# Performance work log

Measured on AMD Instinct MI355X. Metric: run time of the kernel, lower is better.

The kernel has to match this reference:

```python
import jax, jax.numpy as jnp
import numpy as np

B, T, C = 2, 2048, 1024
NH = 16
HD = C // NH

def setup_inputs() -> dict:
    key = jax.random.key(0)
    ks = jax.random.split(key, 4)
    x = jax.random.normal(ks[0], (B, T, C), dtype=jnp.float32)
    w_attn = jax.random.normal(ks[1], (C, 3 * C), dtype=jnp.float32) * (1.0 / np.sqrt(C))
    b_attn = jnp.zeros((3 * C,), dtype=jnp.float32)
    w_proj = jax.random.normal(ks[2], (C, C), dtype=jnp.float32) * (1.0 / np.sqrt(C))
    b_proj = jnp.zeros((C,), dtype=jnp.float32)
    return {"x": x, "w_attn": w_attn, "b_attn": b_attn, "w_proj": w_proj, "b_proj": b_proj}

def reference(x, w_attn, b_attn, w_proj, b_proj):
    Bq, Tq, Cq = x.shape
    qkv = x @ w_attn + b_attn                      # [B,T,3C]
    q, k, v = jnp.split(qkv, 3, axis=2)
    # [B,T,C] -> [B,NH,T,HD]
    def heads(t):
        return t.reshape(Bq, Tq, NH, HD).transpose(0, 2, 1, 3)
    q, k, v = heads(q), heads(k), heads(v)
    att = jnp.einsum('bhqd,bhkd->bhqk', q, k) * (1.0 / np.sqrt(HD))
    causal = jnp.tril(jnp.ones((Tq, Tq), dtype=bool))
    att = jnp.where(causal[None, None], att, -jnp.inf)
    att = jax.nn.softmax(att, axis=-1)
    y = jnp.einsum('bhqk,bhkd->bhqd', att, v)      # [B,NH,T,HD]
    y = y.transpose(0, 2, 1, 3).reshape(Bq, Tq, Cq)
    return y @ w_proj + b_proj
```

## Files before the change

### kernel.cpp

```cpp
#include <hip/hip_runtime.h>

typedef unsigned short u16;
typedef short bf16x8 __attribute__((ext_vector_type(8)));
typedef float f32x4 __attribute__((ext_vector_type(4)));
typedef float f32x16 __attribute__((ext_vector_type(16)));

#define BATCH 2
#define SEQ   2048
#define CH    1024
#define NHEAD 16
#define HDIM  64
#define ROWS  (BATCH*SEQ)

#define WAITV(N) asm volatile("s_waitcnt vmcnt(" #N ")" ::: "memory")

__device__ __forceinline__ u16 f2b(float f) {
  unsigned u = __builtin_bit_cast(unsigned, f);
  u += 0x7FFFu + ((u >> 16) & 1u);
  return (u16)(u >> 16);
}
__device__ __forceinline__ float b2f(u16 h) {
  unsigned u = ((unsigned)h) << 16;
  return __builtin_bit_cast(float, u);
}
__device__ __forceinline__ float exp2_fast(float x) {
  float r; asm("v_exp_f32 %0, %1" : "=v"(r) : "v"(x)); return r;
}
__device__ __forceinline__ unsigned cvt_pk_bf16(float a, float b) {
  unsigned r; asm("v_cvt_pk_bf16_f32 %0, %1, %2" : "=v"(r) : "v"(a), "v"(b)); return r;
}

__device__ __forceinline__ void gload_lds16(const void* g, void* l) {
  __builtin_amdgcn_global_load_lds(
      (const __attribute__((address_space(1))) unsigned int*)g,
      (__attribute__((address_space(3))) unsigned int*)l, 16, 0, 0);
}

__global__ void csa_prep(const float* __restrict__ x,
                         const float* __restrict__ wa, const float* __restrict__ wp,
                         u16* __restrict__ xb, u16* __restrict__ wat,
                         u16* __restrict__ wpt) {
  __shared__ float tile[32][33];
  const int b = blockIdx.x, t = threadIdx.x;
  if (b < 2048) {
    int i = b * 256 + t;
    const float4* f4 = (const float4*)x;
    float4 v0 = f4[2*i], v1 = f4[2*i+1];
    ushort4 o0, o1;
    o0.x = f2b(v0.x); o0.y = f2b(v0.y); o0.z = f2b(v0.z); o0.w = f2b(v0.w);
    o1.x = f2b(v1.x); o1.y = f2b(v1.y); o1.z = f2b(v1.z); o1.w = f2b(v1.w);
    ((ushort4*)xb)[2*i]   = o0;
    ((ushort4*)xb)[2*i+1] = o1;
    return;
  }
  int bb = b - 2048;
  int bx = bb & 127, by = bb >> 7;
  const float* in; u16* out; int C;
  if (bx < 96) { in = wa; out = wat; C = 3*CH; }
  else         { in = wp; out = wpt; C = CH; bx -= 96; }
  const int R = CH;
  const int bxc = bx * 32, byc = by * 32;
  const int tx = t & 31, ty = t >> 5;
  #pragma unroll
  for (int j = 0; j < 4; ++j) {
    int r = byc + ty + j*8, c = bxc + tx;
    tile[ty + j*8][tx] = in[(size_t)r*C + c];
  }
  __syncthreads();
  #pragma unroll
  for (int j = 0; j < 4; ++j) {
    int oc = bxc + ty + j*8;
    int orr = byc + tx;
    out[(size_t)oc*R + orr] = f2b(tile[tx][ty + j*8]);
  }
}

__global__ __launch_bounds__(512) void csa_gemm_qkv(
    const u16* __restrict__ A, const u16* __restrict__ Bt,
    const float* __restrict__ bias,
    u16* __restrict__ qbo, u16* __restrict__ kb, u16* __restrict__ vtb)
{
  __shared__ __align__(16) u16 As[3][256*64];
  __shared__ __align__(16) u16 Bs[2][192*64];
  const int t = threadIdx.x, lane = t & 63, w = t >> 6;
  const int wm = w >> 2, wn = w & 3, g = lane >> 4, qi = lane & 15;
  const int xq = (qi & 7) * 8;

  const int wgid = blockIdx.y * 16 + blockIdx.x;
  const int c8 = wgid & 7, inner = wgid >> 3;
  const int bm = (c8 >> 1) * 4 + (inner >> 3);
  const int bn = (c8 & 1) * 8 + (inner & 7);

  f32x4 acc[8][3] = {};

  const u16* Ab = A  + (size_t)(bm*256)*CH;
  const u16* Bb = Bt + (size_t)(bn*192)*CH;
  const int srow = t >> 3;
  const int scolsw = ((t & 7) * 8) ^ ((srow & 7) * 8);

#define QKV_STAGE_A(kt_, buf_) do { const size_t k_ = (size_t)(kt_)*64;            \
    gload_lds16(Ab + (size_t)(  0 + srow)*CH + k_ + scolsw, &As[buf_][      w*512]); \
    gload_lds16(Ab + (size_t)( 64 + srow)*CH + k_ + scolsw, &As[buf_][ 4096+w*512]); \
    gload_lds16(Ab + (size_t)(128 + srow)*CH + k_ + scolsw, &As[buf_][ 8192+w*512]); \
    gload_lds16(Ab + (size_t)(192 + srow)*CH + k_ + scolsw, &As[buf_][12288+w*512]); \
  } while (0)
#define QKV_STAGE_B(kt_, buf_) do { const size_t k_ = (size_t)(kt_)*64;            \
    gload_lds16(Bb + (size_t)(  0 + srow)*CH + k_ + scolsw, &Bs[buf_][      w*512]); \
    gload_lds16(Bb + (size_t)( 64 + srow)*CH + k_ + scolsw, &Bs[buf_][ 4096+w*512]); \
    gload_lds16(Bb + (size_t)(128 + srow)*CH + k_ + scolsw, &Bs[buf_][ 8192+w*512]); \
  } while (0)

  QKV_STAGE_A(0, 0); QKV_STAGE_B(0, 0); QKV_STAGE_A(1, 1);

  int a3 = 0;
  for (int kt = 0; kt < 16; ++kt) {
    if (kt < 15) QKV_STAGE_B(kt + 1, (kt + 1) & 1);
    if (kt < 14) { int ab = a3 + 2; if (ab >= 3) ab -= 3; QKV_STAGE_A(kt + 2, ab); }
    if (kt < 14)       WAITV(11);
    else if (kt == 14) WAITV(7);
    else               WAITV(0);
    __builtin_amdgcn_s_barrier();
    __builtin_amdgcn_sched_barrier(0);
    const u16* Ac = &As[a3][0];
    const u16* Bc = &Bs[kt & 1][0];
    #pragma unroll
    for (int kk = 0; kk < 2; ++kk) {
      bf16x8 af[8], bfr[3];
      #pragma unroll
      for (int m = 0; m < 8; ++m)
        af[m] = *(const bf16x8*)&Ac[(wm*128 + m*16 + qi)*64 + ((kk*32 + g*8) ^ xq)];
      #pragma unroll
      for (int n = 0; n < 3; ++n)
        bfr[n] = *(const bf16x8*)&Bc[(wn*48 + n*16 + qi)*64 + ((kk*32 + g*8) ^ xq)];
      #pragma unroll
      for (int m = 0; m < 8; ++m)
        #pragma unroll
        for (int n = 0; n < 3; ++n)
          acc[m][n] = __builtin_amdgcn_mfma_f32_16x16x32_bf16(af[m], bfr[n], acc[m][n], 0, 0, 0);
    }
    __builtin_amdgcn_s_barrier();
    a3 = (a3 == 2) ? 0 : a3 + 1;
  }
#undef QKV_STAGE_A
#undef QKV_STAGE_B

  #pragma unroll
  for (int m = 0; m < 8; ++m) {
    const int row0 = bm*256 + wm*128 + m*16 + g*4;
    const int bb = row0 >> 11;
    const int t0 = row0 & 2047;
    #pragma unroll
    for (int n = 0; n < 3; ++n) {
      const int col = bn*192 + wn*48 + n*16 + qi;
      const float bv = bias[col];
      const int which = col >> 10;
      const int cc = col & 1023;
      const int h = cc >> 6, d = cc & 63;
      const int bh = bb*16 + h;
      if (which == 2) {
        ushort4 pw;
        pw.x = f2b(acc[m][n][0] + bv);
        pw.y = f2b(acc[m][n][1] + bv);
        pw.z = f2b(acc[m][n][2] + bv);
        pw.w = f2b(acc[m][n][3] + bv);
        *(ushort4*)&vtb[((size_t)bh*HDIM + d)*SEQ + t0] = pw;
      } else {
        u16* dst = (which == 0) ? qbo : kb;
        #pragma unroll
        for (int r = 0; r < 4; ++r)
          dst[((size_t)bh*SEQ + t0 + r)*HDIM + d] = f2b(acc[m][n][r] + bv);
      }
    }
  }
}

__global__ __launch_bounds__(256) void csa_gemm_proj(
    const u16* __restrict__ A, const u16* __restrict__ Bt,
    const float* __restrict__ bias, float* __restrict__ out)
{
  __shared__ __align__(16) u16 As[3][128*64];
  __shared__ __align__(16) u16 Bs[2][128*64];
  const int t = threadIdx.x, lane = t & 63, w = t >> 6;
  const int wm = w >> 1, wn = w & 1, g = lane >> 4, qi = lane & 15;
  const int xq = (qi & 7) * 8;
  const int bm = blockIdx.y, bn = blockIdx.x;

  f32x4 acc[4][4] = {};

  const u16* Ab = A  + (size_t)(bm*128)*CH;
  const u16* Bb = Bt + (size_t)(bn*128)*CH;
  const int srow = t >> 3;
  const int scolsw = ((t & 7) * 8) ^ ((srow & 7) * 8);

#define PRJ_STAGE(P_, base_, kt_, buf_) do { const size_t k_ = (size_t)(kt_)*64;      \
    gload_lds16(P_ + (size_t)( 0 + srow)*CH + k_ + scolsw, &base_[buf_][     w*512]); \
    gload_lds16(P_ + (size_t)(32 + srow)*CH + k_ + scolsw, &base_[buf_][2048+w*512]); \
    gload_lds16(P_ + (size_t)(64 + srow)*CH + k_ + scolsw, &base_[buf_][4096+w*512]); \
    gload_lds16(P_ + (size_t)(96 + srow)*CH + k_ + scolsw, &base_[buf_][6144+w*512]); \
  } while (0)

  PRJ_STAGE(Ab, As, 0, 0); PRJ_STAGE(Bb, Bs, 0, 0); PRJ_STAGE(Ab, As, 1, 1);

  int a3 = 0;
  for (int kt = 0; kt < 16; ++kt) {
    if (kt < 15) PRJ_STAGE(Bb, Bs, kt + 1, (kt + 1) & 1);
    if (kt < 14) { int ab = a3 + 2; if (ab >= 3) ab -= 3; PRJ_STAGE(Ab, As, kt + 2, ab); }
    if (kt < 14)       WAITV(12);
    else if (kt == 14) WAITV(8);
    else               WAITV(0);
    __builtin_amdgcn_s_barrier();
    __builtin_amdgcn_sched_barrier(0);
    const u16* Ac = &As[a3][0];
    const u16* Bc = &Bs[kt & 1][0];
    #pragma unroll
    for (int kk = 0; kk < 2; ++kk) {
      bf16x8 af[4], bfr[4];
      #pragma unroll
      for (int m = 0; m < 4; ++m)
        af[m] = *(const bf16x8*)&Ac[(wm*64 + m*16 + qi)*64 + ((kk*32 + g*8) ^ xq)];
      #pragma unroll
      for (int n = 0; n < 4; ++n)
        bfr[n] = *(const bf16x8*)&Bc[(wn*64 + n*16 + qi)*64 + ((kk*32 + g*8) ^ xq)];
      #pragma unroll
      for (int m = 0; m < 4; ++m)
        #pragma unroll
        for (int n = 0; n < 4; ++n)
          acc[m][n] = __builtin_amdgcn_mfma_f32_16x16x32_bf16(af[m], bfr[n], acc[m][n], 0, 0, 0);
    }
    __builtin_amdgcn_s_barrier();
    a3 = (a3 == 2) ? 0 : a3 + 1;
  }
#undef PRJ_STAGE

  #pragma unroll
  for (int m = 0; m < 4; ++m) {
    const int row0 = bm*128 + wm*64 + m*16 + g*4;
    #pragma unroll
    for (int n = 0; n < 4; ++n) {
      const int col = bn*128 + wn*64 + n*16 + qi;
      const float bv = bias[col];
      #pragma unroll
      for (int r = 0; r < 4; ++r)
        out[(size_t)(row0 + r)*CH + col] = acc[m][n][r] + bv;
    }
  }
}

__global__ __launch_bounds__(512) void csa_attn(
    const u16* __restrict__ qb, const u16* __restrict__ kb,
    const u16* __restrict__ vtb, u16* __restrict__ yout)
{
  const int bh = blockIdx.x, pair = blockIdx.y;
  const int bidx = bh >> 4, h = bh & 15;
  const int t = threadIdx.x, lane = t & 63, w = t >> 6;
  const int j = w >> 1, sub = w & 1;
  const int l31 = lane & 31, hi = lane >> 5;

  __shared__ __align__(16) u16 Ks[2][128*64];
  __shared__ __align__(16) u16 Vs[2][64*128];
  __shared__ float mtab[8][32], stab[8][32], ftab[8][32];

  const size_t kvbase = (size_t)bh * SEQ * HDIM;
  const u16* kb_bh  = kb  + kvbase;
  const u16* vtb_bh = vtb + kvbase;

  const int krow = t >> 3;
  const int kcol = 8 * ((t & 7) ^ (krow & 7));
  const int vrow = t >> 4;
  const int vcol = 8 * ((t & 15) ^ (vrow & 15));

#define ATTN_STAGE(kt_, b_) do {                                             \
    const u16* kp_ = kb_bh + (size_t)((kt_)*128 + krow)*64 + kcol;           \
    gload_lds16(kp_,           &Ks[b_][       w*512]);                       \
    gload_lds16(kp_ + 64*64,   &Ks[b_][4096 + w*512]);                       \
    const u16* vp_ = vtb_bh + (size_t)vrow*SEQ + (kt_)*128 + vcol;           \
    gload_lds16(vp_,           &Vs[b_][       w*512]);                       \
    gload_lds16(vp_ + 32*SEQ,  &Vs[b_][4096 + w*512]);                       \
  } while (0)

  int offK[2][4];
  #pragma unroll
  for (int kb2 = 0; kb2 < 2; ++kb2)
    #pragma unroll
    for (int ds = 0; ds < 4; ++ds)
      offK[kb2][ds] = (sub*64 + kb2*32 + l31)*64 + ((ds*16 + hi*8) ^ ((l31 & 7)*8));
  int offV[2][4];
  #pragma unroll
  for (int db = 0; db < 2; ++db)
    #pragma unroll
    for (int ks = 0; ks < 4; ++ks)
      offV[db][ks] = (db*32 + l31)*128 + (((sub*8 + 2*ks + hi) ^ (l31 & 15))*8);

#define PACK(ps_, b_, out_) do {                                             \
    unsigned A0_ = cvt_pk_bf16(ps_[(b_)+0], ps_[(b_)+1]);                    \
    unsigned A1_ = cvt_pk_bf16(ps_[(b_)+2], ps_[(b_)+3]);                    \
    unsigned B0_ = cvt_pk_bf16(ps_[(b_)+4], ps_[(b_)+5]);                    \
    unsigned B1_ = cvt_pk_bf16(ps_[(b_)+6], ps_[(b_)+7]);                    \
    asm volatile("v_permlane32_swap_b32 %0, %1" : "+v"(A0_), "+v"(B0_));     \
    asm volatile("v_permlane32_swap_b32 %0, %1" : "+v"(A1_), "+v"(B1_));     \
    union { unsigned u[4]; bf16x8 v; } pu_;                                  \
    pu_.u[0] = A0_; pu_.u[1] = A1_; pu_.u[2] = B0_; pu_.u[3] = B1_;          \
    out_ = pu_.v;                                                            \
  } while (0)

  const float QSCALE = 0.18033688011112042f;
  const int qloc = j*32 + l31;

  for (int half = 0; half < 2; ++half) {
    const int qt = half ? (15 - pair) : pair;
    const int ntile = qt + 1;
    const int qrow = qt*128 + j*32;

    bf16x8 qf[4];
    #pragma unroll
    for (int ds = 0; ds < 4; ++ds) {
      qf[ds] = *(const bf16x8*)&qb[kvbase + (size_t)(qrow + l31)*HDIM + ds*16 + hi*8];
      #pragma unroll
      for (int e = 0; e < 8; ++e)
        qf[ds][e] = (short)f2b(b2f((u16)qf[ds][e]) * QSCALE);
    }

    f32x16 yacc0 = {}, yacc1 = {};
    float mrun = -1e30f, srun = 0.f;

    ATTN_STAGE(0, 0);
    __syncthreads();

    int buf = 0;
    for (int kt = 0; kt < ntile; ++kt) {
      if (kt + 1 < ntile) ATTN_STAGE(kt + 1, buf ^ 1);

      f32x16 s0 = {}, s1 = {};
      #pragma unroll
      for (int ds = 0; ds < 4; ++ds) {
        bf16x8 k0 = *(const bf16x8*)&Ks[buf][offK[0][ds]];
        s0 = __builtin_amdgcn_mfma_f32_32x32x16_bf16(k0, qf[ds], s0, 0, 0, 0);
        bf16x8 k1 = *(const bf16x8*)&Ks[buf][offK[1][ds]];
        s1 = __builtin_amdgcn_mfma_f32_32x32x16_bf16(k1, qf[ds], s1, 0, 0, 0);
      }

      if (kt == ntile - 1) {
        #pragma unroll
        for (int reg = 0; reg < 16; ++reg) {
          const int cr = (reg & 3) + 8*(reg >> 2) + 4*hi;
          if (sub*64 + cr > qloc)      s0[reg] = -3.0e38f;
          if (sub*64 + 32 + cr > qloc) s1[reg] = -3.0e38f;
        }
      }

      float tmax = fmaxf(s0[0], s1[0]);
      #pragma unroll
      for (int reg = 1; reg < 16; ++reg)
        tmax = fmaxf(tmax, fmaxf(s0[reg], s1[reg]));
      if (!__all(tmax - mrun <= 11.5f)) {
        float tmf = fmaxf(tmax, __shfl_xor(tmax, 32));
        float mnew = fmaxf(mrun, tmf);
        float fac = exp2_fast(mrun - mnew);
        if (lane < 32) ftab[w][l31] = fac;
        #pragma unroll
        for (int reg = 0; reg < 16; ++reg) {
          float fr = ftab[w][(reg & 3) + 8*(reg >> 2) + 4*hi];
          yacc0[reg] *= fr; yacc1[reg] *= fr;
        }
        srun *= fac; mrun = mnew;
      }
      float tsum = 0.f;
      #pragma unroll
      for (int reg = 0; reg < 16; ++reg) {
        float p0 = exp2_fast(s0[reg] - mrun);
        float p1 = exp2_fast(s1[reg] - mrun);
        s0[reg] = p0; s1[reg] = p1;
        tsum += p0 + p1;
      }
      srun += tsum;

      bf16x8 pa0, pa1, pa2, pa3;
      PACK(s0, 0, pa0); PACK(s0, 8, pa1); PACK(s1, 0, pa2); PACK(s1, 8, pa3);

      yacc0 = __builtin_amdgcn_mfma_f32_32x32x16_bf16(pa0, *(const bf16x8*)&Vs[buf][offV[0][0]], yacc0, 0, 0, 0);
      yacc0 = __builtin_amdgcn_mfma_f32_32x32x16_bf16(pa1, *(const bf16x8*)&Vs[buf][offV[0][1]], yacc0, 0, 0, 0);
      yacc0 = __builtin_amdgcn_mfma_f32_32x32x16_bf16(pa2, *(const bf16x8*)&Vs[buf][offV[0][2]], yacc0, 0, 0, 0);
      yacc0 = __builtin_amdgcn_mfma_f32_32x32x16_bf16(pa3, *(const bf16x8*)&Vs[buf][offV[0][3]], yacc0, 0, 0, 0);
      yacc1 = __builtin_amdgcn_mfma_f32_32x32x16_bf16(pa0, *(const bf16x8*)&Vs[buf][offV[1][0]], yacc1, 0, 0, 0);
      yacc1 = __builtin_amdgcn_mfma_f32_32x32x16_bf16(pa1, *(const bf16x8*)&Vs[buf][offV[1][1]], yacc1, 0, 0, 0);
      yacc1 = __builtin_amdgcn_mfma_f32_32x32x16_bf16(pa2, *(const bf16x8*)&Vs[buf][offV[1][2]], yacc1, 0, 0, 0);
      yacc1 = __builtin_amdgcn_mfma_f32_32x32x16_bf16(pa3, *(const bf16x8*)&Vs[buf][offV[1][3]], yacc1, 0, 0, 0);

      __syncthreads();
      buf ^= 1;
    }

    float sfull = srun + __shfl_xor(srun, 32);
    if (lane < 32) { mtab[w][l31] = mrun; stab[w][l31] = sfull; }
    __syncthreads();

    float* Ocomb = (float*)&Ks[0][0];
    const int wA = w & ~1, wB = w | 1;
    if (sub == 1) {
      #pragma unroll
      for (int reg = 0; reg < 16; ++reg) {
        const int cr = (reg & 3) + 8*(reg >> 2) + 4*hi;
        float mA = mtab[wA][cr], mB = mtab[wB][cr];
        float fB = exp2_fast(mB - fmaxf(mA, mB));
        Ocomb[(j*32 + cr)*64 +      l31] = yacc0[reg] * fB;
        Ocomb[(j*32 + cr)*64 + 32 + l31] = yacc1[reg] * fB;
      }
    }
    __syncthreads();
    if (sub == 0) {
      #pragma unroll
      for (int reg = 0; reg < 16; ++reg) {
        const int cr = (reg & 3) + 8*(reg >> 2) + 4*hi;
        float mA = mtab[wA][cr], mB = mtab[wB][cr];
        float sA = stab[wA][cr], sB = stab[wB][cr];
        float ms = fmaxf(mA, mB);
        float fA = exp2_fast(mA - ms), fB = exp2_fast(mB - ms);
        float inv = 1.f / (sA * fA + sB * fB);
        const size_t orow = ((size_t)bidx*SEQ + qt*128 + j*32 + cr)*CH + h*HDIM;
        float v0 = (yacc0[reg] * fA + Ocomb[(j*32 + cr)*64 +      l31]) * inv;
        float v1 = (yacc1[reg] * fA + Ocomb[(j*32 + cr)*64 + 32 + l31]) * inv;
        yout[orow +      l31] = f2b(v0);
        yout[orow + 32 + l31] = f2b(v1);
      }
    }
    __syncthreads();
  }
#undef ATTN_STAGE
#undef PACK
}

extern "C" void kernel_launch(void* const* d_in, const int* in_sizes, int n_in,
                              void* d_out, int out_size, void* d_ws, size_t ws_size,
                              hipStream_t stream) {
  (void)in_sizes; (void)n_in; (void)out_size; (void)ws_size;
  const float* x      = (const float*)d_in[0];
  const float* w_attn = (const float*)d_in[1];
  const float* b_attn = (const float*)d_in[2];
  const float* w_proj = (const float*)d_in[3];
  const float* b_proj = (const float*)d_in[4];

  char* ws = (char*)d_ws;
  const size_t MB = 1024*1024;
  u16* xb  = (u16*)(ws);
  u16* wat = (u16*)(ws +  8*MB);
  u16* wpt = (u16*)(ws + 14*MB);
  u16* qb  = (u16*)(ws + 16*MB);
  u16* kb  = (u16*)(ws + 24*MB);
  u16* vtb = (u16*)(ws + 32*MB);

  csa_prep<<<6144, 256, 0, stream>>>(x, w_attn, w_proj, xb, wat, wpt);
  csa_gemm_qkv<<<dim3(16, 16), 512, 0, stream>>>(xb, wat, b_attn, qb, kb, vtb);
  csa_attn<<<dim3(32, 8), 512, 0, stream>>>(qb, kb, vtb, xb);
  csa_gemm_proj<<<dim3(8, 32), 256, 0, stream>>>(xb, wpt, b_proj, (float*)d_out);
}
```

Baseline: 104.9 us.

## Split paired causal query tiles into separate blocks and raise attention occupancy

```diff
diff --git a/kernel.cpp b/kernel.cpp
--- a/kernel.cpp
+++ b/kernel.cpp
@@ -246,11 +246,12 @@
   }
 }
 
-__global__ __launch_bounds__(512) void csa_attn(
+__global__ __launch_bounds__(512, 4) void csa_attn(
     const u16* __restrict__ qb, const u16* __restrict__ kb,
     const u16* __restrict__ vtb, u16* __restrict__ yout)
 {
-  const int bh = blockIdx.x, pair = blockIdx.y;
+  const int bh = blockIdx.x, y = blockIdx.y;
+  const int qt = (y < 8) ? y : 23 - y;
   const int bidx = bh >> 4, h = bh & 15;
   const int t = threadIdx.x, lane = t & 63, w = t >> 6;
   const int j = w >> 1, sub = w & 1;
@@ -305,125 +306,130 @@
 
   const float QSCALE = 0.18033688011112042f;
   const int qloc = j*32 + l31;
-
-  for (int half = 0; half < 2; ++half) {
-    const int qt = half ? (15 - pair) : pair;
-    const int ntile = qt + 1;
-    const int qrow = qt*128 + j*32;
-
-    bf16x8 qf[4];
+  const int ntile = qt + 1;
+  const int qrow = qt*128 + j*32;
+
+  bf16x8 qf[4];
+  #pragma unroll
+  for (int ds = 0; ds < 4; ++ds) {
+    qf[ds] = *(const bf16x8*)&qb[kvbase + (size_t)(qrow + l31)*HDIM + ds*16 + hi*8];
+    #pragma unroll
+    for (int e = 0; e < 8; ++e)
+      qf[ds][e] = (short)f2b(b2f((u16)qf[ds][e]) * QSCALE);
+  }
+
+  f32x16 yacc0 = {}, yacc1 = {};
+  float mrun = -1e30f, srun = 0.f;
+
+  ATTN_STAGE(0, 0);
+  __syncthreads();
+
+  int buf = 0;
+  for (int kt = 0; kt < ntile; ++kt) {
+    if (kt + 1 < ntile) ATTN_STAGE(kt + 1, buf ^ 1);
+
+    f32x16 s0 = {}, s1 = {};
     #pragma unroll
     for (int ds = 0; ds < 4; ++ds) {
-      qf[ds] = *(const bf16x8*)&qb[kvbase + (size_t)(qrow + l31)*HDIM + ds*16 + hi*8];
-      #pragma unroll
-      for (int e = 0; e < 8; ++e)
-        qf[ds][e] = (short)f2b(b2f((u16)qf[ds][e]) * QSCALE);
-    }
-
-    f32x16 yacc0 = {}, yacc1 = {};
-    float mrun = -1e30f, srun = 0.f;
-
-    ATTN_STAGE(0, 0);
-    __syncthreads();
-
-    int buf = 0;
-    for (int kt = 0; kt < ntile; ++kt) {
-      if (kt + 1 < ntile) ATTN_STAGE(kt + 1, buf ^ 1);
-
-      f32x16 s0 = {}, s1 = {};
-      #pragma unroll
-      for (int ds = 0; ds < 4; ++ds) {
-        bf16x8 k0 = *(const bf16x8*)&Ks[buf][offK[0][ds]];
-        s0 = __builtin_amdgcn_mfma_f32_32x32x16_bf16(k0, qf[ds], s0, 0, 0, 0);
-        bf16x8 k1 = *(const bf16x8*)&Ks[buf][offK[1][ds]];
-        s1 = __builtin_amdgcn_mfma_f32_32x32x16_bf16(k1, qf[ds], s1, 0, 0, 0);
-      }
-
-      if (kt == ntile - 1) {
-        #pragma unroll
-        for (int reg = 0; reg < 16; ++reg) {
-          const int cr = (reg & 3) + 8*(reg >> 2) + 4*hi;
-          if (sub*64 + cr > qloc)      s0[reg] = -3.0e38f;
-          if (sub*64 + 32 + cr > qloc) s1[reg] = -3.0e38f;
-        }
-      }
-
-      float tmax = fmaxf(s0[0], s1[0]);
-      #pragma unroll
-      for (int reg = 1; reg < 16; ++reg)
-        tmax = fmaxf(tmax, fmaxf(s0[reg], s1[reg]));
-      if (!__all(tmax - mrun <= 11.5f)) {
-        float tmf = fmaxf(tmax, __shfl_xor(tmax, 32));
-        float mnew = fmaxf(mrun, tmf);
-        float fac = exp2_fast(mrun - mnew);
-        if (lane < 32) ftab[w][l31] = fac;
-        #pragma unroll
-        for (int reg = 0; reg < 16; ++reg) {
-          float fr = ftab[w][(reg & 3) + 8*(reg >> 2) + 4*hi];
-          yacc0[reg] *= fr; yacc1[reg] *= fr;
-        }
-        srun *= fac; mrun = mnew;
-      }
-      float tsum = 0.f;
-      #pragma unroll
-      for (int reg = 0; reg < 16; ++reg) {
-        float p0 = exp2_fast(s0[reg] - mrun);
-        float p1 = exp2_fast(s1[reg] - mrun);
-        s0[reg] = p0; s1[reg] = p1;
-        tsum += p0 + p1;
-      }
-      srun += tsum;
-
-      bf16x8 pa0, pa1, pa2, pa3;
-      PACK(s0, 0, pa0); PACK(s0, 8, pa1); PACK(s1, 0, pa2); PACK(s1, 8, pa3);
-
-      yacc0 = __builtin_amdgcn_mfma_f32_32x32x16_bf16(pa0, *(const bf16x8*)&Vs[buf][offV[0][0]], yacc0, 0, 0, 0);
-      yacc0 = __builtin_amdgcn_mfma_f32_32x32x16_bf16(pa1, *(const bf16x8*)&Vs[buf][offV[0][1]], yacc0, 0, 0, 0);
-      yacc0 = __builtin_amdgcn_mfma_f32_32x32x16_bf16(pa2, *(const bf16x8*)&Vs[buf][offV[0][2]], yacc0, 0, 0, 0);
-      yacc0 = __builtin_amdgcn_mfma_f32_32x32x16_bf16(pa3, *(const bf16x8*)&Vs[buf][offV[0][3]], yacc0, 0, 0, 0);
-      yacc1 = __builtin_amdgcn_mfma_f32_32x32x16_bf16(pa0, *(const bf16x8*)&Vs[buf][offV[1][0]], yacc1, 0, 0, 0);
-      yacc1 = __builtin_amdgcn_mfma_f32_32x32x16_bf16(pa1, *(const bf16x8*)&Vs[buf][offV[1][1]], yacc1, 0, 0, 0);
-      yacc1 = __builtin_amdgcn_mfma_f32_32x32x16_bf16(pa2, *(const bf16x8*)&Vs[buf][offV[1][2]], yacc1, 0, 0, 0);
-      yacc1 = __builtin_amdgcn_mfma_f32_32x32x16_bf16(pa3, *(const bf16x8*)&Vs[buf][offV[1][3]], yacc1, 0, 0, 0);
-
-      __syncthreads();
-      buf ^= 1;
-    }
-
-    float sfull = srun + __shfl_xor(srun, 32);
-    if (lane < 32) { mtab[w][l31] = mrun; stab[w][l31] = sfull; }
-    __syncthreads();
-
-    float* Ocomb = (float*)&Ks[0][0];
-    const int wA = w & ~1, wB = w | 1;
-    if (sub == 1) {
+      bf16x8 k0 = *(const bf16x8*)&Ks[buf][offK[0][ds]];
+      s0 = __builtin_amdgcn_mfma_f32_32x32x16_bf16(k0, qf[ds], s0, 0, 0, 0);
+      bf16x8 k1 = *(const bf16x8*)&Ks[buf][offK[1][ds]];
+      s1 = __builtin_amdgcn_mfma_f32_32x32x16_bf16(k1, qf[ds], s1, 0, 0, 0);
+    }
+
+    if (kt == ntile - 1) {
       #pragma unroll
       for (int reg = 0; reg < 16; ++reg) {
         const int cr = (reg & 3) + 8*(reg >> 2) + 4*hi;
-        float mA = mtab[wA][cr], mB = mtab[wB][cr];
-        float fB = exp2_fast(mB - fmaxf(mA, mB));
-        Ocomb[(j*32 + cr)*64 +      l31] = yacc0[reg] * fB;
-        Ocomb[(j*32 + cr)*64 + 32 + l31] = yacc1[reg] * fB;
+        if (sub*64 + cr > qloc)      s0[reg] = -3.0e38f;
+        if (sub*64 + 32 + cr > qloc) s1[reg] = -3.0e38f;
       }
     }
+
+    float t0 = fmaxf(s0[0], s1[0]), t1 = fmaxf(s0[1], s1[1]);
+    float t2 = fmaxf(s0[2], s1[2]), t3 = fmaxf(s0[3], s1[3]);
+    #pragma unroll
+    for (int reg = 4; reg < 16; reg += 4) {
+      t0 = fmaxf(t0, fmaxf(s0[reg+0], s1[reg+0]));
+      t1 = fmaxf(t1, fmaxf(s0[reg+1], s1[reg+1]));
+      t2 = fmaxf(t2, fmaxf(s0[reg+2], s1[reg+2]));
+      t3 = fmaxf(t3, fmaxf(s0[reg+3], s1[reg+3]));
+    }
+    float tmax = fmaxf(fmaxf(t0, t1), fmaxf(t2, t3));
+    if (!__all(tmax - mrun <= 11.5f)) {
+      float tmf = fmaxf(tmax, __shfl_xor(tmax, 32));
+      float mnew = fmaxf(mrun, tmf);
+      float fac = exp2_fast(mrun - mnew);
+      if (lane < 32) ftab[w][l31] = fac;
+      #pragma unroll
+      for (int reg = 0; reg < 16; ++reg) {
+        float fr = ftab[w][(reg & 3) + 8*(reg >> 2) + 4*hi];
+        yacc0[reg] *= fr; yacc1[reg] *= fr;
+      }
+      srun *= fac; mrun = mnew;
+    }
+    float u0 = 0.f, u1 = 0.f, u2 = 0.f, u3 = 0.f;
+    #pragma unroll
+    for (int reg = 0; reg < 16; reg += 4) {
+      float p00 = exp2_fast(s0[reg+0] - mrun), p10 = exp2_fast(s1[reg+0] - mrun);
+      float p01 = exp2_fast(s0[reg+1] - mrun), p11 = exp2_fast(s1[reg+1] - mrun);
+      float p02 = exp2_fast(s0[reg+2] - mrun), p12 = exp2_fast(s1[reg+2] - mrun);
+      float p03 = exp2_fast(s0[reg+3] - mrun), p13 = exp2_fast(s1[reg+3] - mrun);
+      s0[reg+0] = p00; s1[reg+0] = p10; u0 += p00 + p10;
+      s0[reg+1] = p01; s1[reg+1] = p11; u1 += p01 + p11;
+      s0[reg+2] = p02; s1[reg+2] = p12; u2 += p02 + p12;
+      s0[reg+3] = p03; s1[reg+3] = p13; u3 += p03 + p13;
+    }
+    srun += (u0 + u1) + (u2 + u3);
+
+    bf16x8 pa0, pa1, pa2, pa3;
+    PACK(s0, 0, pa0); PACK(s0, 8, pa1); PACK(s1, 0, pa2); PACK(s1, 8, pa3);
+
+    yacc0 = __builtin_amdgcn_mfma_f32_32x32x16_bf16(pa0, *(const bf16x8*)&Vs[buf][offV[0][0]], yacc0, 0, 0, 0);
+    yacc0 = __builtin_amdgcn_mfma_f32_32x32x16_bf16(pa1, *(const bf16x8*)&Vs[buf][offV[0][1]], yacc0, 0, 0, 0);
+    yacc0 = __builtin_amdgcn_mfma_f32_32x32x16_bf16(pa2, *(const bf16x8*)&Vs[buf][offV[0][2]], yacc0, 0, 0, 0);
+    yacc0 = __builtin_amdgcn_mfma_f32_32x32x16_bf16(pa3, *(const bf16x8*)&Vs[buf][offV[0][3]], yacc0, 0, 0, 0);
+    yacc1 = __builtin_amdgcn_mfma_f32_32x32x16_bf16(pa0, *(const bf16x8*)&Vs[buf][offV[1][0]], yacc1, 0, 0, 0);
+    yacc1 = __builtin_amdgcn_mfma_f32_32x32x16_bf16(pa1, *(const bf16x8*)&Vs[buf][offV[1][1]], yacc1, 0, 0, 0);
+    yacc1 = __builtin_amdgcn_mfma_f32_32x32x16_bf16(pa2, *(const bf16x8*)&Vs[buf][offV[1][2]], yacc1, 0, 0, 0);
+    yacc1 = __builtin_amdgcn_mfma_f32_32x32x16_bf16(pa3, *(const bf16x8*)&Vs[buf][offV[1][3]], yacc1, 0, 0, 0);
+
     __syncthreads();
-    if (sub == 0) {
-      #pragma unroll
-      for (int reg = 0; reg < 16; ++reg) {
-        const int cr = (reg & 3) + 8*(reg >> 2) + 4*hi;
-        float mA = mtab[wA][cr], mB = mtab[wB][cr];
-        float sA = stab[wA][cr], sB = stab[wB][cr];
-        float ms = fmaxf(mA, mB);
-        float fA = exp2_fast(mA - ms), fB = exp2_fast(mB - ms);
-        float inv = 1.f / (sA * fA + sB * fB);
-        const size_t orow = ((size_t)bidx*SEQ + qt*128 + j*32 + cr)*CH + h*HDIM;
-        float v0 = (yacc0[reg] * fA + Ocomb[(j*32 + cr)*64 +      l31]) * inv;
-        float v1 = (yacc1[reg] * fA + Ocomb[(j*32 + cr)*64 + 32 + l31]) * inv;
-        yout[orow +      l31] = f2b(v0);
-        yout[orow + 32 + l31] = f2b(v1);
-      }
-    }
-    __syncthreads();
+    buf ^= 1;
+  }
+
+  float sfull = srun + __shfl_xor(srun, 32);
+  if (lane < 32) { mtab[w][l31] = mrun; stab[w][l31] = sfull; }
+  __syncthreads();
+
+  float* Ocomb = (float*)&Ks[0][0];
+  const int wA = w & ~1, wB = w | 1;
+  if (sub == 1) {
+    #pragma unroll
+    for (int reg = 0; reg < 16; ++reg) {
+      const int cr = (reg & 3) + 8*(reg >> 2) + 4*hi;
+      float mA = mtab[wA][cr], mB = mtab[wB][cr];
+      float fB = exp2_fast(mB - fmaxf(mA, mB));
+      Ocomb[(j*32 + cr)*64 +      l31] = yacc0[reg] * fB;
+      Ocomb[(j*32 + cr)*64 + 32 + l31] = yacc1[reg] * fB;
+    }
+  }
+  __syncthreads();
+  if (sub == 0) {
+    #pragma unroll
+    for (int reg = 0; reg < 16; ++reg) {
+      const int cr = (reg & 3) + 8*(reg >> 2) + 4*hi;
+      float mA = mtab[wA][cr], mB = mtab[wB][cr];
+      float sA = stab[wA][cr], sB = stab[wB][cr];
+      float ms = fmaxf(mA, mB);
+      float fA = exp2_fast(mA - ms), fB = exp2_fast(mB - ms);
+      float inv = 1.f / (sA * fA + sB * fB);
+      const size_t orow = ((size_t)bidx*SEQ + qt*128 + j*32 + cr)*CH + h*HDIM;
+      float v0 = (yacc0[reg] * fA + Ocomb[(j*32 + cr)*64 +      l31]) * inv;
+      float v1 = (yacc1[reg] * fA + Ocomb[(j*32 + cr)*64 + 32 + l31]) * inv;
+      yout[orow +      l31] = f2b(v0);
+      yout[orow + 32 + l31] = f2b(v1);
+    }
   }
 #undef ATTN_STAGE
 #undef PACK
@@ -450,6 +456,6 @@
 
   csa_prep<<<6144, 256, 0, stream>>>(x, w_attn, w_proj, xb, wat, wpt);
   csa_gemm_qkv<<<dim3(16, 16), 512, 0, stream>>>(xb, wat, b_attn, qb, kb, vtb);
-  csa_attn<<<dim3(32, 8), 512, 0, stream>>>(qb, kb, vtb, xb);
+  csa_attn<<<dim3(32, 16), 512, 0, stream>>>(qb, kb, vtb, xb);
   csa_gemm_proj<<<dim3(8, 32), 256, 0, stream>>>(xb, wpt, b_proj, (float*)d_out);
 }
```

Result: faster. 102.8 us (-2.0%).

## Split attention into one q-tile per block and fold max-subtract into MFMA

Applied to the files above, without the earlier changes.

```diff
diff --git a/kernel.cpp b/kernel.cpp
--- a/kernel.cpp
+++ b/kernel.cpp
@@ -246,11 +246,12 @@
   }
 }
 
-__global__ __launch_bounds__(512) void csa_attn(
+__global__ __launch_bounds__(512, 2) void csa_attn(
     const u16* __restrict__ qb, const u16* __restrict__ kb,
     const u16* __restrict__ vtb, u16* __restrict__ yout)
 {
-  const int bh = blockIdx.x, pair = blockIdx.y;
+  const int bh = blockIdx.x, y = blockIdx.y;
+  const int qt = (y < 8) ? y : 23 - y;
   const int bidx = bh >> 4, h = bh & 15;
   const int t = threadIdx.x, lane = t & 63, w = t >> 6;
   const int j = w >> 1, sub = w & 1;
@@ -305,125 +306,148 @@
 
   const float QSCALE = 0.18033688011112042f;
   const int qloc = j*32 + l31;
-
-  for (int half = 0; half < 2; ++half) {
-    const int qt = half ? (15 - pair) : pair;
-    const int ntile = qt + 1;
-    const int qrow = qt*128 + j*32;
-
-    bf16x8 qf[4];
-    #pragma unroll
-    for (int ds = 0; ds < 4; ++ds) {
-      qf[ds] = *(const bf16x8*)&qb[kvbase + (size_t)(qrow + l31)*HDIM + ds*16 + hi*8];
-      #pragma unroll
-      for (int e = 0; e < 8; ++e)
-        qf[ds][e] = (short)f2b(b2f((u16)qf[ds][e]) * QSCALE);
-    }
-
-    f32x16 yacc0 = {}, yacc1 = {};
-    float mrun = -1e30f, srun = 0.f;
-
-    ATTN_STAGE(0, 0);
-    __syncthreads();
-
-    int buf = 0;
-    for (int kt = 0; kt < ntile; ++kt) {
-      if (kt + 1 < ntile) ATTN_STAGE(kt + 1, buf ^ 1);
-
-      f32x16 s0 = {}, s1 = {};
-      #pragma unroll
-      for (int ds = 0; ds < 4; ++ds) {
-        bf16x8 k0 = *(const bf16x8*)&Ks[buf][offK[0][ds]];
-        s0 = __builtin_amdgcn_mfma_f32_32x32x16_bf16(k0, qf[ds], s0, 0, 0, 0);
-        bf16x8 k1 = *(const bf16x8*)&Ks[buf][offK[1][ds]];
-        s1 = __builtin_amdgcn_mfma_f32_32x32x16_bf16(k1, qf[ds], s1, 0, 0, 0);
-      }
-
-      if (kt == ntile - 1) {
-        #pragma unroll
-        for (int reg = 0; reg < 16; ++reg) {
-          const int cr = (reg & 3) + 8*(reg >> 2) + 4*hi;
-          if (sub*64 + cr > qloc)      s0[reg] = -3.0e38f;
-          if (sub*64 + 32 + cr > qloc) s1[reg] = -3.0e38f;
-        }
-      }
-
-      float tmax = fmaxf(s0[0], s1[0]);
-      #pragma unroll
-      for (int reg = 1; reg < 16; ++reg)
-        tmax = fmaxf(tmax, fmaxf(s0[reg], s1[reg]));
-      if (!__all(tmax - mrun <= 11.5f)) {
-        float tmf = fmaxf(tmax, __shfl_xor(tmax, 32));
-        float mnew = fmaxf(mrun, tmf);
-        float fac = exp2_fast(mrun - mnew);
-        if (lane < 32) ftab[w][l31] = fac;
-        #pragma unroll
-        for (int reg = 0; reg < 16; ++reg) {
-          float fr = ftab[w][(reg & 3) + 8*(reg >> 2) + 4*hi];
-          yacc0[reg] *= fr; yacc1[reg] *= fr;
-        }
-        srun *= fac; mrun = mnew;
-      }
-      float tsum = 0.f;
-      #pragma unroll
-      for (int reg = 0; reg < 16; ++reg) {
-        float p0 = exp2_fast(s0[reg] - mrun);
-        float p1 = exp2_fast(s1[reg] - mrun);
-        s0[reg] = p0; s1[reg] = p1;
-        tsum += p0 + p1;
-      }
-      srun += tsum;
-
-      bf16x8 pa0, pa1, pa2, pa3;
-      PACK(s0, 0, pa0); PACK(s0, 8, pa1); PACK(s1, 0, pa2); PACK(s1, 8, pa3);
-
-      yacc0 = __builtin_amdgcn_mfma_f32_32x32x16_bf16(pa0, *(const bf16x8*)&Vs[buf][offV[0][0]], yacc0, 0, 0, 0);
-      yacc0 = __builtin_amdgcn_mfma_f32_32x32x16_bf16(pa1, *(const bf16x8*)&Vs[buf][offV[0][1]], yacc0, 0, 0, 0);
-      yacc0 = __builtin_amdgcn_mfma_f32_32x32x16_bf16(pa2, *(const bf16x8*)&Vs[buf][offV[0][2]], yacc0, 0, 0, 0);
-      yacc0 = __builtin_amdgcn_mfma_f32_32x32x16_bf16(pa3, *(const bf16x8*)&Vs[buf][offV[0][3]], yacc0, 0, 0, 0);
-      yacc1 = __builtin_amdgcn_mfma_f32_32x32x16_bf16(pa0, *(const bf16x8*)&Vs[buf][offV[1][0]], yacc1, 0, 0, 0);
-      yacc1 = __builtin_amdgcn_mfma_f32_32x32x16_bf16(pa1, *(const bf16x8*)&Vs[buf][offV[1][1]], yacc1, 0, 0, 0);
-      yacc1 = __builtin_amdgcn_mfma_f32_32x32x16_bf16(pa2, *(const bf16x8*)&Vs[buf][offV[1][2]], yacc1, 0, 0, 0);
-      yacc1 = __builtin_amdgcn_mfma_f32_32x32x16_bf16(pa3, *(const bf16x8*)&Vs[buf][offV[1][3]], yacc1, 0, 0, 0);
-
-      __syncthreads();
-      buf ^= 1;
-    }
-
-    float sfull = srun + __shfl_xor(srun, 32);
-    if (lane < 32) { mtab[w][l31] = mrun; stab[w][l31] = sfull; }
-    __syncthreads();
-
-    float* Ocomb = (float*)&Ks[0][0];
-    const int wA = w & ~1, wB = w | 1;
-    if (sub == 1) {
+  const int ntile = qt + 1;
+  const int qrow = qt*128 + j*32;
+
+  bf16x8 qf[4];
+  #pragma unroll
+  for (int ds = 0; ds < 4; ++ds) {
+    qf[ds] = *(const bf16x8*)&qb[kvbase + (size_t)(qrow + l31)*HDIM + ds*16 + hi*8];
+    #pragma unroll
+    for (int e = 0; e < 8; ++e)
+      qf[ds][e] = (short)f2b(b2f((u16)qf[ds][e]) * QSCALE);
+  }
+
+  bf16x8 onesb;
+  #pragma unroll
+  for (int e = 0; e < 8; ++e) onesb[e] = (short)0x3F80;
+
+  f32x16 yacc0 = {}, yacc1 = {};
+  f32x16 ones_acc = {};
+  f32x16 msplat = {};
+  float mrun = 0.f;
+
+  ATTN_STAGE(0, 0);
+  __syncthreads();
+
+  int buf = 0;
+  for (int kt = 0; kt < ntile; ++kt) {
+    if (kt + 1 < ntile) ATTN_STAGE(kt + 1, buf ^ 1);
+
+    f32x16 s0, s1;
+    {
+      bf16x8 k00 = *(const bf16x8*)&Ks[buf][offK[0][0]];
+      s0 = __builtin_amdgcn_mfma_f32_32x32x16_bf16(k00, qf[0], msplat, 0, 0, 0);
+      bf16x8 k10 = *(const bf16x8*)&Ks[buf][offK[1][0]];
+      s1 = __builtin_amdgcn_mfma_f32_32x32x16_bf16(k10, qf[0], msplat, 0, 0, 0);
+    }
+    #pragma unroll
+    for (int ds = 1; ds < 4; ++ds) {
+      bf16x8 k0 = *(const bf16x8*)&Ks[buf][offK[0][ds]];
+      s0 = __builtin_amdgcn_mfma_f32_32x32x16_bf16(k0, qf[ds], s0, 0, 0, 0);
+      bf16x8 k1 = *(const bf16x8*)&Ks[buf][offK[1][ds]];
+      s1 = __builtin_amdgcn_mfma_f32_32x32x16_bf16(k1, qf[ds], s1, 0, 0, 0);
+    }
+
+    if (kt == ntile - 1) {
       #pragma unroll
       for (int reg = 0; reg < 16; ++reg) {
         const int cr = (reg & 3) + 8*(reg >> 2) + 4*hi;
-        float mA = mtab[wA][cr], mB = mtab[wB][cr];
-        float fB = exp2_fast(mB - fmaxf(mA, mB));
-        Ocomb[(j*32 + cr)*64 +      l31] = yacc0[reg] * fB;
-        Ocomb[(j*32 + cr)*64 + 32 + l31] = yacc1[reg] * fB;
+        if (sub*64 + cr > qloc)      s0[reg] = -3.0e38f;
+        if (sub*64 + 32 + cr > qloc) s1[reg] = -3.0e38f;
       }
     }
+
+    float a0 = fmaxf(s0[0], s1[0]), a1 = fmaxf(s0[1], s1[1]);
+    float a2 = fmaxf(s0[2], s1[2]), a3 = fmaxf(s0[3], s1[3]);
+    #pragma unroll
+    for (int reg = 4; reg < 16; reg += 4) {
+      a0 = fmaxf(fmaxf(a0, s0[reg+0]), s1[reg+0]);
+      a1 = fmaxf(fmaxf(a1, s0[reg+1]), s1[reg+1]);
+      a2 = fmaxf(fmaxf(a2, s0[reg+2]), s1[reg+2]);
+      a3 = fmaxf(fmaxf(a3, s0[reg+3]), s1[reg+3]);
+    }
+    float tpart = fmaxf(fmaxf(a0, a1), fmaxf(a2, a3));
+    if (!__all(tpart <= 11.5f)) {
+      float tmf = fmaxf(tpart, __shfl_xor(tpart, 32));
+      float delta = fmaxf(tmf, 0.f);
+      float fac = exp2_fast(-delta);
+      if (lane < 32) ftab[w][l31] = fac;
+      #pragma unroll
+      for (int reg = 0; reg < 16; ++reg) {
+        float fr = ftab[w][(reg & 3) + 8*(reg >> 2) + 4*hi];
+        yacc0[reg] *= fr; yacc1[reg] *= fr; ones_acc[reg] *= fr;
+      }
+      mrun += delta;
+      #pragma unroll
+      for (int reg = 0; reg < 16; ++reg) {
+        msplat[reg] = -mrun;
+        s0[reg] -= delta; s1[reg] -= delta;
+      }
+    }
+
+    #pragma unroll
+    for (int reg = 0; reg < 16; ++reg) {
+      s0[reg] = exp2_fast(s0[reg]);
+      s1[reg] = exp2_fast(s1[reg]);
+    }
+
+    bf16x8 pa0, pa1, pa2, pa3;
+    PACK(s0, 0, pa0); PACK(s0, 8, pa1); PACK(s1, 0, pa2); PACK(s1, 8, pa3);
+
+    yacc0 = __builtin_amdgcn_mfma_f32_32x32x16_bf16(pa0, *(const bf16x8*)&Vs[buf][offV[0][0]], yacc0, 0, 0, 0);
+    yacc0 = __builtin_amdgcn_mfma_f32_32x32x16_bf16(pa1, *(const bf16x8*)&Vs[buf][offV[0][1]], yacc0, 0, 0, 0);
+    yacc0 = __builtin_amdgcn_mfma_f32_32x32x16_bf16(pa2, *(const bf16x8*)&Vs[buf][offV[0][2]], yacc0, 0, 0, 0);
+    yacc0 = __builtin_amdgcn_mfma_f32_32x32x16_bf16(pa3, *(const bf16x8*)&Vs[buf][offV[0][3]], yacc0, 0, 0, 0);
+    yacc1 = __builtin_amdgcn_mfma_f32_32x32x16_bf16(pa0, *(const bf16x8*)&Vs[buf][offV[1][0]], yacc1, 0, 0, 0);
+    yacc1 = __builtin_amdgcn_mfma_f32_32x32x16_bf16(pa1, *(const bf16x8*)&Vs[buf][offV[1][1]], yacc1, 0, 0, 0);
+    yacc1 = __builtin_amdgcn_mfma_f32_32x32x16_bf16(pa2, *(const bf16x8*)&Vs[buf][offV[1][2]], yacc1, 0, 0, 0);
+    yacc1 = __builtin_amdgcn_mfma_f32_32x32x16_bf16(pa3, *(const bf16x8*)&Vs[buf][offV[1][3]], yacc1, 0, 0, 0);
+    ones_acc = __builtin_amdgcn_mfma_f32_32x32x16_bf16(pa0, onesb, ones_acc, 0, 0, 0);
+    ones_acc = __builtin_amdgcn_mfma_f32_32x32x16_bf16(pa1, onesb, ones_acc, 0, 0, 0);
+    ones_acc = __builtin_amdgcn_mfma_f32_32x32x16_bf16(pa2, onesb, ones_acc, 0, 0, 0);
+    ones_acc = __builtin_amdgcn_mfma_f32_32x32x16_bf16(pa3, onesb, ones_acc, 0, 0, 0);
+
     __syncthreads();
-    if (sub == 0) {
-      #pragma unroll
-      for (int reg = 0; reg < 16; ++reg) {
-        const int cr = (reg & 3) + 8*(reg >> 2) + 4*hi;
-        float mA = mtab[wA][cr], mB = mtab[wB][cr];
-        float sA = stab[wA][cr], sB = stab[wB][cr];
-        float ms = fmaxf(mA, mB);
-        float fA = exp2_fast(mA - ms), fB = exp2_fast(mB - ms);
-        float inv = 1.f / (sA * fA + sB * fB);
-        const size_t orow = ((size_t)bidx*SEQ + qt*128 + j*32 + cr)*CH + h*HDIM;
-        float v0 = (yacc0[reg] * fA + Ocomb[(j*32 + cr)*64 +      l31]) * inv;
-        float v1 = (yacc1[reg] * fA + Ocomb[(j*32 + cr)*64 + 32 + l31]) * inv;
-        yout[orow +      l31] = f2b(v0);
-        yout[orow + 32 + l31] = f2b(v1);
-      }
-    }
-    __syncthreads();
+    buf ^= 1;
+  }
+
+  if (lane < 32) mtab[w][l31] = mrun;
+  if (l31 == 0) {
+    #pragma unroll
+    for (int reg = 0; reg < 16; ++reg)
+      stab[w][(reg & 3) + 8*(reg >> 2) + 4*hi] = ones_acc[reg];
+  }
+  __syncthreads();
+
+  float* Ocomb = (float*)&Ks[0][0];
+  const int wA = w & ~1, wB = w | 1;
+  if (sub == 1) {
+    #pragma unroll
+    for (int reg = 0; reg < 16; ++reg) {
+      const int cr = (reg & 3) + 8*(reg >> 2) + 4*hi;
+      float mA = mtab[wA][cr], mB = mtab[wB][cr];
+      float fB = exp2_fast(mB - fmaxf(mA, mB));
+      Ocomb[(j*32 + cr)*64 +      l31] = yacc0[reg] * fB;
+      Ocomb[(j*32 + cr)*64 + 32 + l31] = yacc1[reg] * fB;
+    }
+  }
+  __syncthreads();
+  if (sub == 0) {
+    #pragma unroll
+    for (int reg = 0; reg < 16; ++reg) {
+      const int cr = (reg & 3) + 8*(reg >> 2) + 4*hi;
+      float mA = mtab[wA][cr], mB = mtab[wB][cr];
+      float sA = stab[wA][cr], sB = stab[wB][cr];
+      float ms = fmaxf(mA, mB);
+      float fA = exp2_fast(mA - ms), fB = exp2_fast(mB - ms);
+      float inv = 1.f / (sA * fA + sB * fB);
+      const size_t orow = ((size_t)bidx*SEQ + qt*128 + j*32 + cr)*CH + h*HDIM;
+      float v0 = (yacc0[reg] * fA + Ocomb[(j*32 + cr)*64 +      l31]) * inv;
+      float v1 = (yacc1[reg] * fA + Ocomb[(j*32 + cr)*64 + 32 + l31]) * inv;
+      yout[orow +      l31] = f2b(v0);
+      yout[orow + 32 + l31] = f2b(v1);
+    }
   }
 #undef ATTN_STAGE
 #undef PACK
@@ -450,6 +474,6 @@
 
   csa_prep<<<6144, 256, 0, stream>>>(x, w_attn, w_proj, xb, wat, wpt);
   csa_gemm_qkv<<<dim3(16, 16), 512, 0, stream>>>(xb, wat, b_attn, qb, kb, vtb);
-  csa_attn<<<dim3(32, 8), 512, 0, stream>>>(qb, kb, vtb, xb);
+  csa_attn<<<dim3(32, 16), 512, 0, stream>>>(qb, kb, vtb, xb);
   csa_gemm_proj<<<dim3(8, 32), 256, 0, stream>>>(xb, wpt, b_proj, (float*)d_out);
 }
```

After: 102.5 us. 2.3% less time.

## Rewrite attention kernel to register-resident K/V with per-wave causal chunks

Applied to the files above, without the earlier changes.

```diff
diff --git a/kernel.cpp b/kernel.cpp
--- a/kernel.cpp
+++ b/kernel.cpp
@@ -246,50 +246,55 @@
   }
 }
 
-__global__ __launch_bounds__(512) void csa_attn(
+__global__ __launch_bounds__(256, 3) void csa_attn(
     const u16* __restrict__ qb, const u16* __restrict__ kb,
     const u16* __restrict__ vtb, u16* __restrict__ yout)
 {
-  const int bh = blockIdx.x, pair = blockIdx.y;
+  const int bh = blockIdx.x, qt = 15 - blockIdx.y;
   const int bidx = bh >> 4, h = bh & 15;
-  const int t = threadIdx.x, lane = t & 63, w = t >> 6;
-  const int j = w >> 1, sub = w & 1;
+  const int t = threadIdx.x, lane = t & 63, j = t >> 6;
   const int l31 = lane & 31, hi = lane >> 5;
 
-  __shared__ __align__(16) u16 Ks[2][128*64];
-  __shared__ __align__(16) u16 Vs[2][64*128];
-  __shared__ float mtab[8][32], stab[8][32], ftab[8][32];
-
   const size_t kvbase = (size_t)bh * SEQ * HDIM;
-  const u16* kb_bh  = kb  + kvbase;
-  const u16* vtb_bh = vtb + kvbase;
-
-  const int krow = t >> 3;
-  const int kcol = 8 * ((t & 7) ^ (krow & 7));
-  const int vrow = t >> 4;
-  const int vcol = 8 * ((t & 15) ^ (vrow & 15));
-
-#define ATTN_STAGE(kt_, b_) do {                                             \
-    const u16* kp_ = kb_bh + (size_t)((kt_)*128 + krow)*64 + kcol;           \
-    gload_lds16(kp_,           &Ks[b_][       w*512]);                       \
-    gload_lds16(kp_ + 64*64,   &Ks[b_][4096 + w*512]);                       \
-    const u16* vp_ = vtb_bh + (size_t)vrow*SEQ + (kt_)*128 + vcol;           \
-    gload_lds16(vp_,           &Vs[b_][       w*512]);                       \
-    gload_lds16(vp_ + 32*SEQ,  &Vs[b_][4096 + w*512]);                       \
+  const u16* kb_bh = kb + kvbase;
+  const u16* vt0 = vtb + kvbase + (size_t)l31 * SEQ;
+  const u16* vt1 = vt0 + (size_t)32 * SEQ;
+  const int qrow = qt*128 + j*32;
+  const int nch = 4*qt + j + 1;
+
+  const float QSCALE = 0.18033688011112042f;
+
+  bf16x8 qf[4];
+  #pragma unroll
+  for (int ds = 0; ds < 4; ++ds) {
+    qf[ds] = *(const bf16x8*)&qb[kvbase + (size_t)(qrow + l31)*HDIM + ds*16 + hi*8];
+    #pragma unroll
+    for (int e = 0; e < 8; ++e)
+      qf[ds][e] = (short)f2b(b2f((u16)qf[ds][e]) * QSCALE);
+  }
+
+  bf16x8 onesb;
+  #pragma unroll
+  for (int e = 0; e < 8; ++e) onesb[e] = (short)0x3F80;
+
+  f32x16 yacc0 = {}, yacc1 = {};
+  f32x16 ones_acc = {};
+  float mrun = 0.f;
+
+  const int koff = hi*8;
+
+  bf16x8 kf[4], vf0[2], vf1[2];
+  bf16x8 knx[4], vnx0[2], vnx1[2];
+
+#define LOAD_CHUNK(kb_, KF, VF0, VF1) do {                                       \
+    const u16* kp_ = kb_bh + (size_t)((kb_) + l31)*HDIM + koff;                  \
+    KF[0] = *(const bf16x8*)(kp_);        KF[1] = *(const bf16x8*)(kp_ + 16);    \
+    KF[2] = *(const bf16x8*)(kp_ + 32);   KF[3] = *(const bf16x8*)(kp_ + 48);    \
+    VF0[0] = *(const bf16x8*)&vt0[(kb_) + koff];                                 \
+    VF0[1] = *(const bf16x8*)&vt0[(kb_) + 16 + koff];                            \
+    VF1[0] = *(const bf16x8*)&vt1[(kb_) + koff];                                 \
+    VF1[1] = *(const bf16x8*)&vt1[(kb_) + 16 + koff];                            \
   } while (0)
-
-  int offK[2][4];
-  #pragma unroll
-  for (int kb2 = 0; kb2 < 2; ++kb2)
-    #pragma unroll
-    for (int ds = 0; ds < 4; ++ds)
-      offK[kb2][ds] = (sub*64 + kb2*32 + l31)*64 + ((ds*16 + hi*8) ^ ((l31 & 7)*8));
-  int offV[2][4];
-  #pragma unroll
-  for (int db = 0; db < 2; ++db)
-    #pragma unroll
-    for (int ks = 0; ks < 4; ++ks)
-      offV[db][ks] = (db*32 + l31)*128 + (((sub*8 + 2*ks + hi) ^ (l31 & 15))*8);
 
 #define PACK(ps_, b_, out_) do {                                             \
     unsigned A0_ = cvt_pk_bf16(ps_[(b_)+0], ps_[(b_)+1]);                    \
@@ -303,129 +308,74 @@
     out_ = pu_.v;                                                            \
   } while (0)
 
-  const float QSCALE = 0.18033688011112042f;
-  const int qloc = j*32 + l31;
-
-  for (int half = 0; half < 2; ++half) {
-    const int qt = half ? (15 - pair) : pair;
-    const int ntile = qt + 1;
-    const int qrow = qt*128 + j*32;
-
-    bf16x8 qf[4];
-    #pragma unroll
-    for (int ds = 0; ds < 4; ++ds) {
-      qf[ds] = *(const bf16x8*)&qb[kvbase + (size_t)(qrow + l31)*HDIM + ds*16 + hi*8];
-      #pragma unroll
-      for (int e = 0; e < 8; ++e)
-        qf[ds][e] = (short)f2b(b2f((u16)qf[ds][e]) * QSCALE);
-    }
-
-    f32x16 yacc0 = {}, yacc1 = {};
-    float mrun = -1e30f, srun = 0.f;
-
-    ATTN_STAGE(0, 0);
-    __syncthreads();
-
-    int buf = 0;
-    for (int kt = 0; kt < ntile; ++kt) {
-      if (kt + 1 < ntile) ATTN_STAGE(kt + 1, buf ^ 1);
-
-      f32x16 s0 = {}, s1 = {};
-      #pragma unroll
-      for (int ds = 0; ds < 4; ++ds) {
-        bf16x8 k0 = *(const bf16x8*)&Ks[buf][offK[0][ds]];
-        s0 = __builtin_amdgcn_mfma_f32_32x32x16_bf16(k0, qf[ds], s0, 0, 0, 0);
-        bf16x8 k1 = *(const bf16x8*)&Ks[buf][offK[1][ds]];
-        s1 = __builtin_amdgcn_mfma_f32_32x32x16_bf16(k1, qf[ds], s1, 0, 0, 0);
-      }
-
-      if (kt == ntile - 1) {
-        #pragma unroll
-        for (int reg = 0; reg < 16; ++reg) {
-          const int cr = (reg & 3) + 8*(reg >> 2) + 4*hi;
-          if (sub*64 + cr > qloc)      s0[reg] = -3.0e38f;
-          if (sub*64 + 32 + cr > qloc) s1[reg] = -3.0e38f;
-        }
-      }
-
-      float tmax = fmaxf(s0[0], s1[0]);
-      #pragma unroll
-      for (int reg = 1; reg < 16; ++reg)
-        tmax = fmaxf(tmax, fmaxf(s0[reg], s1[reg]));
-      if (!__all(tmax - mrun <= 11.5f)) {
-        float tmf = fmaxf(tmax, __shfl_xor(tmax, 32));
-        float mnew = fmaxf(mrun, tmf);
-        float fac = exp2_fast(mrun - mnew);
-        if (lane < 32) ftab[w][l31] = fac;
-        #pragma unroll
-        for (int reg = 0; reg < 16; ++reg) {
-          float fr = ftab[w][(reg & 3) + 8*(reg >> 2) + 4*hi];
-          yacc0[reg] *= fr; yacc1[reg] *= fr;
-        }
-        srun *= fac; mrun = mnew;
-      }
-      float tsum = 0.f;
-      #pragma unroll
-      for (int reg = 0; reg < 16; ++reg) {
-        float p0 = exp2_fast(s0[reg] - mrun);
-        float p1 = exp2_fast(s1[reg] - mrun);
-        s0[reg] = p0; s1[reg] = p1;
-        tsum += p0 + p1;
-      }
-      srun += tsum;
-
-      bf16x8 pa0, pa1, pa2, pa3;
-      PACK(s0, 0, pa0); PACK(s0, 8, pa1); PACK(s1, 0, pa2); PACK(s1, 8, pa3);
-
-      yacc0 = __builtin_amdgcn_mfma_f32_32x32x16_bf16(pa0, *(const bf16x8*)&Vs[buf][offV[0][0]], yacc0, 0, 0, 0);
-      yacc0 = __builtin_amdgcn_mfma_f32_32x32x16_bf16(pa1, *(const bf16x8*)&Vs[buf][offV[0][1]], yacc0, 0, 0, 0);
-      yacc0 = __builtin_amdgcn_mfma_f32_32x32x16_bf16(pa2, *(const bf16x8*)&Vs[buf][offV[0][2]], yacc0, 0, 0, 0);
-      yacc0 = __builtin_amdgcn_mfma_f32_32x32x16_bf16(pa3, *(const bf16x8*)&Vs[buf][offV[0][3]], yacc0, 0, 0, 0);
-      yacc1 = __builtin_amdgcn_mfma_f32_32x32x16_bf16(pa0, *(const bf16x8*)&Vs[buf][offV[1][0]], yacc1, 0, 0, 0);
-      yacc1 = __builtin_amdgcn_mfma_f32_32x32x16_bf16(pa1, *(const bf16x8*)&Vs[buf][offV[1][1]], yacc1, 0, 0, 0);
-      yacc1 = __builtin_amdgcn_mfma_f32_32x32x16_bf16(pa2, *(const bf16x8*)&Vs[buf][offV[1][2]], yacc1, 0, 0, 0);
-      yacc1 = __builtin_amdgcn_mfma_f32_32x32x16_bf16(pa3, *(const bf16x8*)&Vs[buf][offV[1][3]], yacc1, 0, 0, 0);
-
-      __syncthreads();
-      buf ^= 1;
-    }
-
-    float sfull = srun + __shfl_xor(srun, 32);
-    if (lane < 32) { mtab[w][l31] = mrun; stab[w][l31] = sfull; }
-    __syncthreads();
-
-    float* Ocomb = (float*)&Ks[0][0];
-    const int wA = w & ~1, wB = w | 1;
-    if (sub == 1) {
+  LOAD_CHUNK(0, kf, vf0, vf1);
+
+  for (int ch = 0; ch < nch; ++ch) {
+    if (ch + 1 < nch) LOAD_CHUNK((ch + 1)*32, knx, vnx0, vnx1);
+
+    f32x16 s = {};
+    #pragma unroll
+    for (int ds = 0; ds < 4; ++ds)
+      s = __builtin_amdgcn_mfma_f32_32x32x16_bf16(kf[ds], qf[ds], s, 0, 0, 0);
+
+    if (ch == nch - 1) {
       #pragma unroll
       for (int reg = 0; reg < 16; ++reg) {
         const int cr = (reg & 3) + 8*(reg >> 2) + 4*hi;
-        float mA = mtab[wA][cr], mB = mtab[wB][cr];
-        float fB = exp2_fast(mB - fmaxf(mA, mB));
-        Ocomb[(j*32 + cr)*64 +      l31] = yacc0[reg] * fB;
-        Ocomb[(j*32 + cr)*64 + 32 + l31] = yacc1[reg] * fB;
+        if (cr > l31) s[reg] = -3.0e38f;
       }
     }
-    __syncthreads();
-    if (sub == 0) {
+
+    float a0 = fmaxf(s[0], s[1]),  a1 = fmaxf(s[2], s[3]);
+    float a2 = fmaxf(s[4], s[5]),  a3 = fmaxf(s[6], s[7]);
+    #pragma unroll
+    for (int reg = 8; reg < 16; reg += 4) {
+      a0 = fmaxf(fmaxf(a0, s[reg+0]), s[reg+1]);
+      a2 = fmaxf(fmaxf(a2, s[reg+2]), s[reg+3]);
+    }
+    float tmax = fmaxf(fmaxf(a0, a1), fmaxf(a2, a3));
+    if (!__all(tmax - mrun <= 11.5f)) {
+      float tmf = fmaxf(tmax, __shfl_xor(tmax, 32));
+      float mnew = fmaxf(mrun, tmf);
+      float fac = exp2_fast(mrun - mnew);
       #pragma unroll
       for (int reg = 0; reg < 16; ++reg) {
         const int cr = (reg & 3) + 8*(reg >> 2) + 4*hi;
-        float mA = mtab[wA][cr], mB = mtab[wB][cr];
-        float sA = stab[wA][cr], sB = stab[wB][cr];
-        float ms = fmaxf(mA, mB);
-        float fA = exp2_fast(mA - ms), fB = exp2_fast(mB - ms);
-        float inv = 1.f / (sA * fA + sB * fB);
-        const size_t orow = ((size_t)bidx*SEQ + qt*128 + j*32 + cr)*CH + h*HDIM;
-        float v0 = (yacc0[reg] * fA + Ocomb[(j*32 + cr)*64 +      l31]) * inv;
-        float v1 = (yacc1[reg] * fA + Ocomb[(j*32 + cr)*64 + 32 + l31]) * inv;
-        yout[orow +      l31] = f2b(v0);
-        yout[orow + 32 + l31] = f2b(v1);
+        float fr = __shfl(fac, cr);
+        yacc0[reg] *= fr; yacc1[reg] *= fr; ones_acc[reg] *= fr;
       }
-    }
-    __syncthreads();
-  }
-#undef ATTN_STAGE
+      mrun = mnew;
+    }
+
+    #pragma unroll
+    for (int reg = 0; reg < 16; ++reg)
+      s[reg] = exp2_fast(s[reg] - mrun);
+
+    bf16x8 pa0, pa1;
+    PACK(s, 0, pa0); PACK(s, 8, pa1);
+
+    yacc0 = __builtin_amdgcn_mfma_f32_32x32x16_bf16(pa0, vf0[0], yacc0, 0, 0, 0);
+    yacc0 = __builtin_amdgcn_mfma_f32_32x32x16_bf16(pa1, vf0[1], yacc0, 0, 0, 0);
+    yacc1 = __builtin_amdgcn_mfma_f32_32x32x16_bf16(pa0, vf1[0], yacc1, 0, 0, 0);
+    yacc1 = __builtin_amdgcn_mfma_f32_32x32x16_bf16(pa1, vf1[1], yacc1, 0, 0, 0);
+    ones_acc = __builtin_amdgcn_mfma_f32_32x32x16_bf16(pa0, onesb, ones_acc, 0, 0, 0);
+    ones_acc = __builtin_amdgcn_mfma_f32_32x32x16_bf16(pa1, onesb, ones_acc, 0, 0, 0);
+
+    #pragma unroll
+    for (int ds = 0; ds < 4; ++ds) kf[ds] = knx[ds];
+    vf0[0] = vnx0[0]; vf0[1] = vnx0[1];
+    vf1[0] = vnx1[0]; vf1[1] = vnx1[1];
+  }
+
+  #pragma unroll
+  for (int reg = 0; reg < 16; ++reg) {
+    const int cr = (reg & 3) + 8*(reg >> 2) + 4*hi;
+    float inv = 1.f / ones_acc[reg];
+    const size_t orow = ((size_t)bidx*SEQ + qrow + cr)*CH + h*HDIM;
+    yout[orow +      l31] = f2b(yacc0[reg] * inv);
+    yout[orow + 32 + l31] = f2b(yacc1[reg] * inv);
+  }
+#undef LOAD_CHUNK
 #undef PACK
 }
 
@@ -450,6 +400,6 @@
 
   csa_prep<<<6144, 256, 0, stream>>>(x, w_attn, w_proj, xb, wat, wpt);
   csa_gemm_qkv<<<dim3(16, 16), 512, 0, stream>>>(xb, wat, b_attn, qb, kb, vtb);
-  csa_attn<<<dim3(32, 8), 512, 0, stream>>>(qb, kb, vtb, xb);
+  csa_attn<<<dim3(32, 16), 256, 0, stream>>>(qb, kb, vtb, xb);
   csa_gemm_proj<<<dim3(8, 32), 256, 0, stream>>>(xb, wpt, b_proj, (float*)d_out);
 }
```

Result: slower. 151.8 us (+44.7%).
